# Performance work log

Hardware: AMD Instinct MI355X
Metric: run time of the kernel (lower is better)

The kernel has to match this reference:

```python
import jax, jax.numpy as jnp
import numpy as np

N_A, N_G, D, H = 100000, 25000, 128, 4
E_B, E_O, E_R, E_P = 400000, 100000, 200000, 200000
BN_INV = float(1.0 / np.sqrt(1.0 + 1e-5))  # eval-mode BatchNorm1d, running mean 0 / var 1


def setup_inputs():
    key = jax.random.key(0)
    ks = iter(jax.random.split(key, 64))
    nrm = lambda shape, s=0.05: jax.random.normal(next(ks), shape, jnp.float32) * s
    ri = lambda n, hi: jax.random.randint(next(ks), (n,), 0, hi, jnp.int32)
    inp = dict(
        x_atom=nrm((N_A, D), 1.0), x_group=nrm((N_G, D), 1.0),
        ef_bond=nrm((E_B, D), 1.0), ef_overlap=nrm((E_O, D), 1.0),
        bond_src=ri(E_B, N_A), bond_dst=ri(E_B, N_A),
        ov_src=ri(E_O, N_G), ov_dst=ri(E_O, N_G),
        ref_src=ri(E_R, N_G), ref_dst=ri(E_R, N_A),
        pool_src=ri(E_P, N_A), pool_dst=ri(E_P, N_G),
    )
    # two GINE convs (bond 'b', overlap 'o'): eps + MLP Linear(D,2D)->BN->ReLU->Linear(2D,D)
    for pre in ('b', 'o'):
        inp[pre + '_eps'] = jnp.zeros((1,), jnp.float32)
        inp[pre + '_W1'] = nrm((D, 2 * D)); inp[pre + '_b1'] = jnp.zeros((2 * D,), jnp.float32)
        inp[pre + '_g1'] = jnp.ones((2 * D,), jnp.float32); inp[pre + '_be1'] = jnp.zeros((2 * D,), jnp.float32)
        inp[pre + '_W2'] = nrm((2 * D, D)); inp[pre + '_b2'] = jnp.zeros((D,), jnp.float32)
    # two ModifiedGATConvs (refine 'r', pool 'p'): GATConv + Flatten->BN->ReLU->Linear
    for pre in ('r', 'p'):
        inp[pre + '_Wfc'] = nrm((D, H * D)); inp[pre + '_al'] = nrm((H, D)); inp[pre + '_ar'] = nrm((H, D))
        inp[pre + '_Wres'] = nrm((D, H * D)); inp[pre + '_bias'] = jnp.zeros((H * D,), jnp.float32)
        inp[pre + '_g'] = jnp.ones((H * D,), jnp.float32); inp[pre + '_b'] = jnp.zeros((H * D,), jnp.float32)
        inp[pre + '_Wout'] = nrm((H * D, D)); inp[pre + '_bout'] = jnp.zeros((D,), jnp.float32)
    return inp


def _gine(x_src, x_dst, efeat, src, dst, n_dst, eps, W1, b1, g1, be1, W2, b2):
    m = jax.nn.relu(x_src[src] + efeat)                       # [E, D] message: relu(h_src + e)
    neigh = jax.ops.segment_sum(m, dst, num_segments=n_dst)   # [Nd, D] sum-reduce
    h = (1.0 + eps) * x_dst + neigh
    h = h @ W1 + b1
    h = jax.nn.relu(g1 * (h * BN_INV) + be1)                  # eval BN
    return h @ W2 + b2


def _gat(x_src, x_dst, src, dst, n_dst, Wfc, al, ar, Wres, bias, g, b, Wout, bout):
    hs = (x_src @ Wfc).reshape(-1, H, D)                      # [Ns, H, D]
    hd = (x_dst @ Wfc).reshape(-1, H, D)
    el = jnp.sum(hs * al, axis=-1)                            # [Ns, H]
    er = jnp.sum(hd * ar, axis=-1)                            # [Nd, H]
    e = jax.nn.leaky_relu(el[src] + er[dst], 0.2)             # [E, H]
    emax = jax.ops.segment_max(e, dst, num_segments=n_dst)    # per-dst softmax (stable)
    ex = jnp.exp(e - emax[dst])
    den = jax.ops.segment_sum(ex, dst, num_segments=n_dst)
    a = ex / jnp.maximum(den[dst], 1e-9)                      # [E, H]
    rst = jax.ops.segment_sum(a[:, :, None] * hs[src], dst, num_segments=n_dst)  # [Nd, H, D]
    rst = rst + (x_dst @ Wres).reshape(-1, H, D) + bias.reshape(H, D)            # residual + bias
    flat = rst.reshape(-1, H * D)                             # Flatten
    h = jax.nn.relu(g * (flat * BN_INV) + b)                  # eval BN -> ReLU
    return h @ Wout + bout


def reference(x_atom, x_group, ef_bond, ef_overlap, bond_src, bond_dst, ov_src, ov_dst, ref_src, ref_dst, pool_src, pool_dst, b_eps, b_W1, b_b1, b_g1, b_be1, b_W2, b_b2, o_eps, o_W1, o_b1, o_g1, o_be1, o_W2, o_b2, r_Wfc, r_al, r_ar, r_Wres, r_bias, r_g, r_b, r_Wout, r_bout, p_Wfc, p_al, p_ar, p_Wres, p_bias, p_g, p_b, p_Wout, p_bout):
    # HeteroGraphConv with default 'sum' cross-relation aggregation per dst node type
    out_atom = _gine(x_atom, x_atom, ef_bond, bond_src, bond_dst, N_A, b_eps, b_W1, b_b1, b_g1, b_be1, b_W2, b_b2)
    out_atom = out_atom + _gat(x_group, x_atom, ref_src, ref_dst, N_A, r_Wfc, r_al, r_ar, r_Wres, r_bias, r_g, r_b, r_Wout, r_bout)
    out_group = _gine(x_group, x_group, ef_overlap, ov_src, ov_dst, N_G, o_eps, o_W1, o_b1, o_g1, o_be1, o_W2, o_b2)
    out_group = out_group + _gat(x_atom, x_group, pool_src, pool_dst, N_G, p_Wfc, p_al, p_ar, p_Wres, p_bias, p_g, p_b, p_Wout, p_bout)
    return jnp.concatenate([out_atom, out_group], axis=0)     # [N_A + N_G, D]
```

## Files before the change

kernel.cpp:

```cpp
#include <hip/hip_runtime.h>
#include <hip/hip_bf16.h>

#define N_A 100000
#define N_G 25000
#define DD 128
#define E_B 400000
#define E_O 100000
#define E_R 200000
#define E_P 200000
#define EALL 900000
#define NSLOT 250000
#define STRIDE 64

static constexpr float BN_INV_C = 0.99999500003749969f;

typedef __attribute__((ext_vector_type(8))) short bf16x8;
typedef __attribute__((ext_vector_type(4))) float f32x4;

__device__ __forceinline__ unsigned short f2bf(float f) {
    unsigned u = __float_as_uint(f);
    unsigned r = (u + 0x7FFFu + ((u >> 16) & 1u)) >> 16;
    return (unsigned short)r;
}
__device__ __forceinline__ float bf2f(unsigned short s) {
    return __uint_as_float(((unsigned)s) << 16);
}
__device__ __forceinline__ float lrelu(float v) { return v > 0.f ? v : 0.2f * v; }

__global__ void k_xcast_all(const float* __restrict__ xa, const float* __restrict__ xg,
                            unsigned short* __restrict__ xab, unsigned short* __restrict__ xgb) {
    int t = blockIdx.x * blockDim.x + threadIdx.x;
    if (t < N_A * 32) {
        float4 v = *(const float4*)(xa + (size_t)t * 4);
        ushort4 o; o.x = f2bf(v.x); o.y = f2bf(v.y); o.z = f2bf(v.z); o.w = f2bf(v.w);
        *(ushort4*)(xab + (size_t)t * 4) = o;
    } else {
        int t2 = t - N_A * 32;
        if (t2 >= N_G * 32) return;
        float4 v = *(const float4*)(xg + (size_t)t2 * 4);
        ushort4 o; o.x = f2bf(v.x); o.y = f2bf(v.y); o.z = f2bf(v.z); o.w = f2bf(v.w);
        *(ushort4*)(xgb + (size_t)t2 * 4) = o;
    }
}

struct WcSeg { const float* src; unsigned short* dst; int K; int N; int ldk; int off; };
struct WcArgs { WcSeg s[10]; };

__global__ void k_wcast_all(WcArgs a) {
    WcSeg sg = a.s[blockIdx.y];
    int t = blockIdx.x * blockDim.x + threadIdx.x;
    if (t >= sg.K * sg.N) return;
    int n = t % sg.N, k = t / sg.N;
    sg.dst[(size_t)n * sg.ldk + sg.off + k] = f2bf(sg.src[t]);
}

__global__ void k_war_all(const float* __restrict__ rWfc, const float* __restrict__ ral,
                          const float* __restrict__ rar, const float* __restrict__ pWfc,
                          const float* __restrict__ pal, const float* __restrict__ par,
                          float* __restrict__ wv) {
    int bsel = blockIdx.x;
    const float* W = bsel < 2 ? rWfc : pWfc;
    const float* vec = bsel == 0 ? ral : bsel == 1 ? rar : bsel == 2 ? pal : par;
    float* o = wv + bsel * 512;
    int t = threadIdx.x;
    int k = t >> 2, h = t & 3;
    const float* wr = W + (size_t)k * 512 + h * 128;
    const float* av = vec + h * 128;
    float s = 0.f;
    for (int d = 0; d < 128; ++d) s += wr[d] * av[d];
    o[t] = s;
}

__global__ void k_adj_fill(const int* __restrict__ bs, const int* __restrict__ bd,
                           const int* __restrict__ os, const int* __restrict__ od,
                           const int* __restrict__ rs, const int* __restrict__ rd,
                           const int* __restrict__ ps, const int* __restrict__ pd,
                           int* __restrict__ deg, uint2* __restrict__ adj,
                           int* __restrict__ heads, int* __restrict__ nxt) {
    int t = blockIdx.x * blockDim.x + threadIdx.x;
    int e, base, go; const int* S; const int* D;
    if (t < E_B) { e = t; S = bs; D = bd; base = 0; go = 0; }
    else if (t < E_B + E_O) { e = t - E_B; S = os; D = od; base = 100000; go = E_B; }
    else if (t < E_B + E_O + E_R) { e = t - (E_B + E_O); S = rs; D = rd; base = 125000; go = E_B + E_O; }
    else if (t < EALL) { e = t - (E_B + E_O + E_R); S = ps; D = pd; base = 225000; go = E_B + E_O + E_R; }
    else return;
    int d = D[e], s = S[e];
    int ns = base + d;
    int pos = atomicAdd(&deg[ns], 1);
    if (pos < STRIDE) adj[(size_t)ns * STRIDE + pos] = make_uint2((unsigned)e, (unsigned)s);
    else nxt[go + e] = atomicExch(&heads[ns], e);
}

__global__ __launch_bounds__(256) void k_gine_gather_all(
    const unsigned short* __restrict__ xAb, const unsigned short* __restrict__ xGb,
    const float* __restrict__ efB, const float* __restrict__ efO,
    const int* __restrict__ bsrc, const int* __restrict__ osrc,
    const int* __restrict__ deg, const uint2* __restrict__ adj,
    const int* __restrict__ heads, const int* __restrict__ nxt,
    const float* __restrict__ beps, const float* __restrict__ oeps,
    unsigned short* __restrict__ h0A, unsigned short* __restrict__ h0G) {
    int wid = threadIdx.x >> 6, lane = threadIdx.x & 63;
    int n = blockIdx.x * 4 + wid;
    __shared__ uint2 gl[4][STRIDE];
    const unsigned short* xs; const unsigned short* xdrow; const float* ef;
    const int* esrc; const int* nx; float ep; unsigned short* outp; int nn, base, go;
    if (n < N_A) {
        nn = n; xs = xAb; xdrow = xAb + (size_t)n * DD; ef = efB; esrc = bsrc;
        base = 0; go = 0; ep = 1.0f + beps[0]; outp = h0A + (size_t)n * DD;
    } else {
        nn = n - N_A; xs = xGb; xdrow = xGb + (size_t)nn * DD; ef = efO; esrc = osrc;
        base = 100000; go = E_B; ep = 1.0f + oeps[0]; outp = h0G + (size_t)nn * DD;
    }
    nx = nxt + go;
    int d = deg[base + nn];
    int cb = min(d, STRIDE);
    if (lane < cb) gl[wid][lane] = adj[(size_t)(base + nn) * STRIDE + lane];
    __syncthreads();
    float2 acc = make_float2(0.f, 0.f);
    for (int i = 0; i < cb; ++i) {
        uint2 es = gl[wid][i];
        unsigned xa = *(const unsigned*)(xs + (size_t)es.y * DD + lane * 2);
        float2 ev = *(const float2*)(ef + (size_t)es.x * DD + lane * 2);
        acc.x += fmaxf(bf2f((unsigned short)(xa & 0xffff)) + ev.x, 0.f);
        acc.y += fmaxf(bf2f((unsigned short)(xa >> 16)) + ev.y, 0.f);
    }
    if (d > STRIDE) {
        for (int e = heads[base + nn]; e >= 0; e = nx[e]) {
            int s = esrc[e];
            unsigned xa = *(const unsigned*)(xs + (size_t)s * DD + lane * 2);
            float2 ev = *(const float2*)(ef + (size_t)e * DD + lane * 2);
            acc.x += fmaxf(bf2f((unsigned short)(xa & 0xffff)) + ev.x, 0.f);
            acc.y += fmaxf(bf2f((unsigned short)(xa >> 16)) + ev.y, 0.f);
        }
    }
    unsigned xd = *(const unsigned*)(xdrow + lane * 2);
    float rx = ep * bf2f((unsigned short)(xd & 0xffff)) + acc.x;
    float ry = ep * bf2f((unsigned short)(xd >> 16)) + acc.y;
    *(unsigned*)(outp + lane * 2) = (unsigned)f2bf(rx) | ((unsigned)f2bf(ry) << 16);
}

__global__ void k_logit_all(const unsigned short* __restrict__ xAb,
                            const unsigned short* __restrict__ xGb,
                            const float* __restrict__ wv,
                            float* __restrict__ elR, float* __restrict__ elP,
                            float* __restrict__ erR, float* __restrict__ erP) {
    int t = blockIdx.x * blockDim.x + threadIdx.x;
    const unsigned short* xr; const float* wl; const float* wr_; float* ol; float* orr; int idx;
    if (t < N_A * 4) {
        idx = t; xr = xAb + (size_t)(t >> 2) * DD; wl = wv + 1024; wr_ = wv + 512;
        ol = elP; orr = erR;
    } else {
        int t2 = t - N_A * 4;
        if (t2 >= N_G * 4) return;
        idx = t2; xr = xGb + (size_t)(t2 >> 2) * DD; wl = wv; wr_ = wv + 1536;
        ol = elR; orr = erP;
    }
    int h = idx & 3;
    float sl = 0.f, sr = 0.f;
#pragma unroll
    for (int k = 0; k < DD; k += 8) {
        uint4 w = *(const uint4*)(xr + k);
        unsigned wa[4] = {w.x, w.y, w.z, w.w};
#pragma unroll
        for (int q = 0; q < 4; ++q) {
            float x0 = bf2f((unsigned short)(wa[q] & 0xffff));
            float x1 = bf2f((unsigned short)(wa[q] >> 16));
            int k0 = (k + q * 2) * 4 + h, k1 = (k + q * 2 + 1) * 4 + h;
            sl += x0 * wl[k0] + x1 * wl[k1];
            sr += x0 * wr_[k0] + x1 * wr_[k1];
        }
    }
    ol[idx] = sl;
    orr[idx] = sr;
}

__global__ void k_exp_all(const float* __restrict__ elR, const float* __restrict__ erR,
                          const float* __restrict__ elP, const float* __restrict__ erP,
                          const int* __restrict__ rs, const int* __restrict__ rd,
                          const int* __restrict__ ps, const int* __restrict__ pd,
                          float* __restrict__ exR, float* __restrict__ exP,
                          float* __restrict__ denR, float* __restrict__ denP) {
    int t = blockIdx.x * blockDim.x + threadIdx.x;
    if (t < E_R * 4) {
        int e = t >> 2, h = t & 3;
        float v = lrelu(elR[rs[e] * 4 + h] + erR[rd[e] * 4 + h]);
        float x = __expf(v);
        exR[t] = x;
        atomicAdd(&denR[rd[e] * 4 + h], x);
    } else {
        int t2 = t - E_R * 4;
        if (t2 >= E_P * 4) return;
        int e = t2 >> 2, h = t2 & 3;
        float v = lrelu(elP[ps[e] * 4 + h] + erP[pd[e] * 4 + h]);
        float x = __expf(v);
        exP[t2] = x;
        atomicAdd(&denP[pd[e] * 4 + h], x);
    }
}

__global__ __launch_bounds__(256) void k_att_gather_all(
    const unsigned short* __restrict__ xAb, const unsigned short* __restrict__ xGb,
    const float* __restrict__ exR, const float* __restrict__ exP,
    const float* __restrict__ denR, const float* __restrict__ denP,
    const int* __restrict__ rsrc, const int* __restrict__ psrc,
    const int* __restrict__ deg, const uint2* __restrict__ adj,
    const int* __restrict__ heads, const int* __restrict__ nxt,
    unsigned short* __restrict__ A2r, unsigned short* __restrict__ A2p) {
    int wid = threadIdx.x >> 6, lane = threadIdx.x & 63;
    int n = blockIdx.x * 4 + wid;
    __shared__ uint2 gl[4][STRIDE];
    const unsigned short* xs; const float* ex; const float* den;
    const int* esrc; const int* nx; unsigned short* A2; int nn, base, go;
    if (n < N_A) {
        nn = n; xs = xGb; ex = exR; den = denR; esrc = rsrc;
        base = 125000; go = E_B + E_O; A2 = A2r + (size_t)n * 512;
    } else {
        nn = n - N_A; xs = xAb; ex = exP; den = denP; esrc = psrc;
        base = 225000; go = E_B + E_O + E_R; A2 = A2p + (size_t)nn * 512;
    }
    nx = nxt + go;
    int d = deg[base + nn];
    int cb = min(d, STRIDE);
    if (lane < cb) gl[wid][lane] = adj[(size_t)(base + nn) * STRIDE + lane];
    __syncthreads();
    float4 dv = *(const float4*)(den + (size_t)nn * 4);
    float inv0 = 1.f / fmaxf(dv.x, 1e-9f);
    float inv1 = 1.f / fmaxf(dv.y, 1e-9f);
    float inv2 = 1.f / fmaxf(dv.z, 1e-9f);
    float inv3 = 1.f / fmaxf(dv.w, 1e-9f);
    float acc[4][2] = {};
    for (int i = 0; i < cb; ++i) {
        uint2 es = gl[wid][i];
        float4 e4 = *(const float4*)(ex + (size_t)es.x * 4);
        unsigned xw = *(const unsigned*)(xs + (size_t)es.y * DD + lane * 2);
        float x0 = bf2f((unsigned short)(xw & 0xffff));
        float x1 = bf2f((unsigned short)(xw >> 16));
        float a0 = e4.x * inv0, a1 = e4.y * inv1, a2 = e4.z * inv2, a3 = e4.w * inv3;
        acc[0][0] += a0 * x0; acc[0][1] += a0 * x1;
        acc[1][0] += a1 * x0; acc[1][1] += a1 * x1;
        acc[2][0] += a2 * x0; acc[2][1] += a2 * x1;
        acc[3][0] += a3 * x0; acc[3][1] += a3 * x1;
    }
    if (d > STRIDE) {
        for (int e = heads[base + nn]; e >= 0; e = nx[e]) {
            int s = esrc[e];
            float4 e4 = *(const float4*)(ex + (size_t)e * 4);
            unsigned xw = *(const unsigned*)(xs + (size_t)s * DD + lane * 2);
            float x0 = bf2f((unsigned short)(xw & 0xffff));
            float x1 = bf2f((unsigned short)(xw >> 16));
            float a0 = e4.x * inv0, a1 = e4.y * inv1, a2 = e4.z * inv2, a3 = e4.w * inv3;
            acc[0][0] += a0 * x0; acc[0][1] += a0 * x1;
            acc[1][0] += a1 * x0; acc[1][1] += a1 * x1;
            acc[2][0] += a2 * x0; acc[2][1] += a2 * x1;
            acc[3][0] += a3 * x0; acc[3][1] += a3 * x1;
        }
    }
#pragma unroll
    for (int h = 0; h < 4; ++h) {
        unsigned o = (unsigned)f2bf(acc[h][0]) | ((unsigned)f2bf(acc[h][1]) << 16);
        *(unsigned*)(A2 + h * 128 + lane * 2) = o;
    }
}

#define LDKP 40
template <int EPI, int OUTBF, int GATK>
__global__ __launch_bounds__(256) void k_gemm_bf(
    const unsigned short* __restrict__ A, const unsigned short* __restrict__ Bt,
    void* __restrict__ C, int M, int N, int K,
    const float* __restrict__ bias, const float* __restrict__ g,
    const float* __restrict__ be, const unsigned short* __restrict__ addbf,
    const unsigned short* __restrict__ Axd) {
    __shared__ unsigned short As[128 * LDKP];
    __shared__ unsigned short Bs[128 * LDKP];
    int tid = threadIdx.x;
    int wave = tid >> 6, lane = tid & 63;
    int wr = wave >> 1, wc = wave & 1;
    int row0 = blockIdx.y * 128, col0 = blockIdx.x * 128;
    int l16 = lane & 15, khalf = (lane >> 4) * 8;
    f32x4 acc[4][4] = {};
    int r_0 = tid >> 2, ko_0 = (tid & 3) * 8;
    int r_1 = (tid + 256) >> 2, ko_1 = ((tid + 256) & 3) * 8;
    for (int k0 = 0; k0 < K; k0 += 32) {
        __syncthreads();
        {
            int kk = k0 + ko_0;
            int ra = min(row0 + r_0, M - 1);
            uint4 va;
            if (GATK) va = (kk < 128) ? *(const uint4*)(A + (size_t)ra * 512 + col0 + kk)
                                      : *(const uint4*)(Axd + (size_t)ra * 128 + (kk - 128));
            else va = *(const uint4*)(A + (size_t)ra * K + kk);
            *(uint4*)(&As[r_0 * LDKP + ko_0]) = va;
            uint4 vb = *(const uint4*)(Bt + (size_t)(col0 + r_0) * K + kk);
            *(uint4*)(&Bs[r_0 * LDKP + ko_0]) = vb;
            kk = k0 + ko_1;
            ra = min(row0 + r_1, M - 1);
            if (GATK) va = (kk < 128) ? *(const uint4*)(A + (size_t)ra * 512 + col0 + kk)
                                      : *(const uint4*)(Axd + (size_t)ra * 128 + (kk - 128));
            else va = *(const uint4*)(A + (size_t)ra * K + kk);
            *(uint4*)(&As[r_1 * LDKP + ko_1]) = va;
            vb = *(const uint4*)(Bt + (size_t)(col0 + r_1) * K + kk);
            *(uint4*)(&Bs[r_1 * LDKP + ko_1]) = vb;
        }
        __syncthreads();
        bf16x8 af[4], bfr[4];
#pragma unroll
        for (int i = 0; i < 4; ++i)
            af[i] = *(const bf16x8*)(&As[(wr * 64 + i * 16 + l16) * LDKP + khalf]);
#pragma unroll
        for (int j = 0; j < 4; ++j)
            bfr[j] = *(const bf16x8*)(&Bs[(wc * 64 + j * 16 + l16) * LDKP + khalf]);
#pragma unroll
        for (int i = 0; i < 4; ++i)
#pragma unroll
            for (int j = 0; j < 4; ++j)
                acc[i][j] = __builtin_amdgcn_mfma_f32_16x16x32_bf16(af[i], bfr[j], acc[i][j], 0, 0, 0);
    }
    int rq = (lane >> 4) * 4;
#pragma unroll
    for (int i = 0; i < 4; ++i) {
#pragma unroll
        for (int reg = 0; reg < 4; ++reg) {
            int r = row0 + wr * 64 + i * 16 + rq + reg;
            if (r >= M) continue;
#pragma unroll
            for (int j = 0; j < 4; ++j) {
                int c = col0 + wc * 64 + j * 16 + l16;
                float v = acc[i][j][reg];
                size_t idx = (size_t)r * N + c;
                v += bias[c];
                if (EPI == 2) {
                    v = g[c] * (v * BN_INV_C) + be[c];
                    v = fmaxf(v, 0.f);
                }
                if (EPI == 3) {
                    ((float*)C)[idx] = v + bf2f(addbf[idx]);
                } else if (OUTBF) {
                    ((unsigned short*)C)[idx] = f2bf(v);
                } else {
                    ((float*)C)[idx] = v;
                }
            }
        }
    }
}

extern "C" void kernel_launch(void* const* d_in, const int* in_sizes, int n_in,
                              void* d_out, int out_size, void* d_ws, size_t ws_size,
                              hipStream_t stream) {
    const float* x_atom = (const float*)d_in[0];
    const float* x_group = (const float*)d_in[1];
    const float* ef_bond = (const float*)d_in[2];
    const float* ef_ov = (const float*)d_in[3];
    const int* bond_src = (const int*)d_in[4];
    const int* bond_dst = (const int*)d_in[5];
    const int* ov_src = (const int*)d_in[6];
    const int* ov_dst = (const int*)d_in[7];
    const int* ref_src = (const int*)d_in[8];
    const int* ref_dst = (const int*)d_in[9];
    const int* pool_src = (const int*)d_in[10];
    const int* pool_dst = (const int*)d_in[11];
    const float* b_eps = (const float*)d_in[12];
    const float* b_W1 = (const float*)d_in[13];
    const float* b_b1 = (const float*)d_in[14];
    const float* b_g1 = (const float*)d_in[15];
    const float* b_be1 = (const float*)d_in[16];
    const float* b_W2 = (const float*)d_in[17];
    const float* b_b2 = (const float*)d_in[18];
    const float* o_eps = (const float*)d_in[19];
    const float* o_W1 = (const float*)d_in[20];
    const float* o_b1 = (const float*)d_in[21];
    const float* o_g1 = (const float*)d_in[22];
    const float* o_be1 = (const float*)d_in[23];
    const float* o_W2 = (const float*)d_in[24];
    const float* o_b2 = (const float*)d_in[25];
    const float* r_Wfc = (const float*)d_in[26];
    const float* r_al = (const float*)d_in[27];
    const float* r_ar = (const float*)d_in[28];
    const float* r_Wres = (const float*)d_in[29];
    const float* r_bias = (const float*)d_in[30];
    const float* r_g = (const float*)d_in[31];
    const float* r_b = (const float*)d_in[32];
    const float* r_Wout = (const float*)d_in[33];
    const float* r_bout = (const float*)d_in[34];
    const float* p_Wfc = (const float*)d_in[35];
    const float* p_al = (const float*)d_in[36];
    const float* p_ar = (const float*)d_in[37];
    const float* p_Wres = (const float*)d_in[38];
    const float* p_bias = (const float*)d_in[39];
    const float* p_g = (const float*)d_in[40];
    const float* p_b = (const float*)d_in[41];
    const float* p_Wout = (const float*)d_in[42];
    const float* p_bout = (const float*)d_in[43];

    float* out = (float*)d_out;
    char* wsb = (char*)d_ws;
    unsigned short* xAb = (unsigned short*)(wsb + 0);
    unsigned short* xGb = (unsigned short*)(wsb + 26000000);
    unsigned short* WtB1 = (unsigned short*)(wsb + 33000000);
    unsigned short* WtB2 = WtB1 + 32768;
    unsigned short* WtO1 = WtB2 + 32768;
    unsigned short* WtO2 = WtO1 + 32768;
    unsigned short* WtR  = WtO2 + 32768;
    unsigned short* WtRo = WtR + 131072;
    unsigned short* WtP  = WtRo + 65536;
    unsigned short* WtPo = WtP + 131072;
    float* wv   = (float*)(wsb + 34100000);
    int* heads  = (int*)(wsb + 36300000);
    int* nxt    = (int*)(wsb + 37400000);
    unsigned short* h0A = (unsigned short*)(wsb + 41100000);
    unsigned short* h0G = (unsigned short*)(wsb + 66800000);
    unsigned short* R4  = (unsigned short*)(wsb + 73300000);
    unsigned short* G1a = (unsigned short*)(wsb + 124600000);
    unsigned short* G1g = (unsigned short*)(wsb + 150300000);
    unsigned short* A2r = (unsigned short*)(wsb + 156800000);
    unsigned short* A2p = (unsigned short*)(wsb + 259300000);
    unsigned short* R3r = (unsigned short*)(wsb + 285000000);
    unsigned short* R3p = (unsigned short*)(wsb + 387500000);
    uint2* adj  = (uint2*)(wsb + 414000000);
    int* deg    = (int*)(wsb + 543000000);
    float* F    = (float*)(wsb + 544000000);
    float* elR  = F;
    float* elP  = F + 100000;
    float* erR  = F + 500000;
    float* erP  = F + 900000;
    float* denR = F + 1000000;
    float* denP = F + 1400000;
    float* exR  = F + 1500000;
    float* exP  = F + 2300000;

    k_xcast_all<<<((N_A + N_G) * 32 + 255) / 256, 256, 0, stream>>>(x_atom, x_group, xAb, xGb);
    WcArgs wa;
    wa.s[0] = {b_W1, WtB1, 128, 256, 128, 0};
    wa.s[1] = {b_W2, WtB2, 256, 128, 256, 0};
    wa.s[2] = {o_W1, WtO1, 128, 256, 128, 0};
    wa.s[3] = {o_W2, WtO2, 256, 128, 256, 0};
    wa.s[4] = {r_Wfc, WtR, 128, 512, 256, 0};
    wa.s[5] = {r_Wres, WtR, 128, 512, 256, 128};
    wa.s[6] = {r_Wout, WtRo, 512, 128, 512, 0};
    wa.s[7] = {p_Wfc, WtP, 128, 512, 256, 0};
    wa.s[8] = {p_Wres, WtP, 128, 512, 256, 128};
    wa.s[9] = {p_Wout, WtPo, 512, 128, 512, 0};
    k_wcast_all<<<dim3(256, 10), 256, 0, stream>>>(wa);
    k_war_all<<<4, 512, 0, stream>>>(r_Wfc, r_al, r_ar, p_Wfc, p_al, p_ar, wv);
    hipMemsetAsync(deg, 0, NSLOT * 4, stream);
    hipMemsetAsync(heads, 0xFF, NSLOT * 4, stream);
    hipMemsetAsync(denR, 0, 500000 * 4, stream);
    k_adj_fill<<<(EALL + 255) / 256, 256, 0, stream>>>(
        bond_src, bond_dst, ov_src, ov_dst, ref_src, ref_dst, pool_src, pool_dst,
        deg, adj, heads, nxt);
    k_gine_gather_all<<<31250, 256, 0, stream>>>(xAb, xGb, ef_bond, ef_ov, bond_src, ov_src,
                                                 deg, adj, heads, nxt, b_eps, o_eps, h0A, h0G);
    k_gemm_bf<2, 1, 0><<<dim3(2, 782), 256, 0, stream>>>(h0A, WtB1, R4, N_A, 256, 128, b_b1, b_g1, b_be1, nullptr, nullptr);
    k_gemm_bf<1, 1, 0><<<dim3(1, 782), 256, 0, stream>>>(R4, WtB2, G1a, N_A, 128, 256, b_b2, nullptr, nullptr, nullptr, nullptr);
    k_gemm_bf<2, 1, 0><<<dim3(2, 196), 256, 0, stream>>>(h0G, WtO1, R4, N_G, 256, 128, o_b1, o_g1, o_be1, nullptr, nullptr);
    k_gemm_bf<1, 1, 0><<<dim3(1, 196), 256, 0, stream>>>(R4, WtO2, G1g, N_G, 128, 256, o_b2, nullptr, nullptr, nullptr, nullptr);
    k_logit_all<<<((N_A + N_G) * 4 + 255) / 256, 256, 0, stream>>>(xAb, xGb, wv, elR, elP, erR, erP);
    k_exp_all<<<((E_R + E_P) * 4 + 255) / 256, 256, 0, stream>>>(elR, erR, elP, erP,
        ref_src, ref_dst, pool_src, pool_dst, exR, exP, denR, denP);
    k_att_gather_all<<<31250, 256, 0, stream>>>(xAb, xGb, exR, exP, denR, denP, ref_src, pool_src,
                                                deg, adj, heads, nxt, A2r, A2p);
    k_gemm_bf<2, 1, 1><<<dim3(4, 782), 256, 0, stream>>>(A2r, WtR, R3r, N_A, 512, 256, r_bias, r_g, r_b, nullptr, xAb);
    k_gemm_bf<2, 1, 1><<<dim3(4, 196), 256, 0, stream>>>(A2p, WtP, R3p, N_G, 512, 256, p_bias, p_g, p_b, nullptr, xGb);
    k_gemm_bf<3, 0, 0><<<dim3(1, 782), 256, 0, stream>>>(R3r, WtRo, out, N_A, 128, 512, r_bout, nullptr, nullptr, G1a, nullptr);
    k_gemm_bf<3, 0, 0><<<dim3(1, 196), 256, 0, stream>>>(R3p, WtPo, out + (size_t)N_A * DD, N_G, 128, 512, p_bout, nullptr, nullptr, G1g, nullptr);
}
```

Measured before the change: 596.8 us.

## Merge independent kernels into fewer grouped launches and batch GEMMs

Combines the casting, weight transpose, attention-vector precompute and adjacency fill into one prep kernel, fuses the GINE gather with the logit computation, and groups the GEMMs into three launches that dispatch sub-problems by block index. A separate R4g buffer lets the group-side GEMMs run alongside the atom-side ones. The aim is to cut launch count and fill tail idle time. The cost is heavier kernels with more branching, and possibly higher register pressure from the shared gemm_body.

Measured after the change: 542.3 us. -9.1%, faster.

```diff
diff --git a/kernel.cpp b/kernel.cpp
--- a/kernel.cpp
+++ b/kernel.cpp
@@ -27,151 +27,156 @@
 }
 __device__ __forceinline__ float lrelu(float v) { return v > 0.f ? v : 0.2f * v; }
 
-__global__ void k_xcast_all(const float* __restrict__ xa, const float* __restrict__ xg,
-                            unsigned short* __restrict__ xab, unsigned short* __restrict__ xgb) {
-    int t = blockIdx.x * blockDim.x + threadIdx.x;
-    if (t < N_A * 32) {
-        float4 v = *(const float4*)(xa + (size_t)t * 4);
-        ushort4 o; o.x = f2bf(v.x); o.y = f2bf(v.y); o.z = f2bf(v.z); o.w = f2bf(v.w);
-        *(ushort4*)(xab + (size_t)t * 4) = o;
+struct WcSeg { const float* src; unsigned short* dst; int K; int N; int ldk; int off; };
+struct PrepArgs {
+    const float* xa; const float* xg;
+    unsigned short* xab; unsigned short* xgb;
+    WcSeg wc[10];
+    const float* rWfc; const float* ral; const float* rar;
+    const float* pWfc; const float* pal; const float* par;
+    float* wv;
+    const int* bs; const int* bd; const int* os; const int* od;
+    const int* rs; const int* rd; const int* ps; const int* pd;
+    int* deg; uint2* adj; int* heads; int* nxt;
+};
+
+#define PB_XC 15625
+#define PB_WC 2560
+#define PB_WAR 8
+
+__global__ __launch_bounds__(256) void k_prep(PrepArgs p) {
+    int bx = blockIdx.x, tid = threadIdx.x;
+    if (bx < PB_XC) {
+        int t = bx * 256 + tid;
+        if (t < N_A * 32) {
+            float4 v = *(const float4*)(p.xa + (size_t)t * 4);
+            ushort4 o; o.x = f2bf(v.x); o.y = f2bf(v.y); o.z = f2bf(v.z); o.w = f2bf(v.w);
+            *(ushort4*)(p.xab + (size_t)t * 4) = o;
+        } else {
+            int t2 = t - N_A * 32;
+            if (t2 < N_G * 32) {
+                float4 v = *(const float4*)(p.xg + (size_t)t2 * 4);
+                ushort4 o; o.x = f2bf(v.x); o.y = f2bf(v.y); o.z = f2bf(v.z); o.w = f2bf(v.w);
+                *(ushort4*)(p.xgb + (size_t)t2 * 4) = o;
+            }
+        }
+    } else if (bx < PB_XC + PB_WC) {
+        int b2 = bx - PB_XC;
+        WcSeg sg = p.wc[b2 >> 8];
+        int t = ((b2 & 255) << 8) + tid;
+        if (t < sg.K * sg.N) {
+            int n = t % sg.N, k = t / sg.N;
+            sg.dst[(size_t)n * sg.ldk + sg.off + k] = f2bf(sg.src[t]);
+        }
+    } else if (bx < PB_XC + PB_WC + PB_WAR) {
+        int b3 = bx - (PB_XC + PB_WC);
+        int bsel = b3 >> 1;
+        int t = ((b3 & 1) << 8) + tid;
+        const float* W = bsel < 2 ? p.rWfc : p.pWfc;
+        const float* vec = bsel == 0 ? p.ral : bsel == 1 ? p.rar : bsel == 2 ? p.pal : p.par;
+        int k = t >> 2, h = t & 3;
+        const float* wr = W + (size_t)k * 512 + h * 128;
+        const float* av = vec + h * 128;
+        float s = 0.f;
+        for (int d = 0; d < 128; ++d) s += wr[d] * av[d];
+        p.wv[bsel * 512 + t] = s;
     } else {
-        int t2 = t - N_A * 32;
-        if (t2 >= N_G * 32) return;
-        float4 v = *(const float4*)(xg + (size_t)t2 * 4);
-        ushort4 o; o.x = f2bf(v.x); o.y = f2bf(v.y); o.z = f2bf(v.z); o.w = f2bf(v.w);
-        *(ushort4*)(xgb + (size_t)t2 * 4) = o;
-    }
-}
-
-struct WcSeg { const float* src; unsigned short* dst; int K; int N; int ldk; int off; };
-struct WcArgs { WcSeg s[10]; };
-
-__global__ void k_wcast_all(WcArgs a) {
-    WcSeg sg = a.s[blockIdx.y];
-    int t = blockIdx.x * blockDim.x + threadIdx.x;
-    if (t >= sg.K * sg.N) return;
-    int n = t % sg.N, k = t / sg.N;
-    sg.dst[(size_t)n * sg.ldk + sg.off + k] = f2bf(sg.src[t]);
-}
-
-__global__ void k_war_all(const float* __restrict__ rWfc, const float* __restrict__ ral,
-                          const float* __restrict__ rar, const float* __restrict__ pWfc,
-                          const float* __restrict__ pal, const float* __restrict__ par,
-                          float* __restrict__ wv) {
-    int bsel = blockIdx.x;
-    const float* W = bsel < 2 ? rWfc : pWfc;
-    const float* vec = bsel == 0 ? ral : bsel == 1 ? rar : bsel == 2 ? pal : par;
-    float* o = wv + bsel * 512;
-    int t = threadIdx.x;
-    int k = t >> 2, h = t & 3;
-    const float* wr = W + (size_t)k * 512 + h * 128;
-    const float* av = vec + h * 128;
-    float s = 0.f;
-    for (int d = 0; d < 128; ++d) s += wr[d] * av[d];
-    o[t] = s;
-}
-
-__global__ void k_adj_fill(const int* __restrict__ bs, const int* __restrict__ bd,
-                           const int* __restrict__ os, const int* __restrict__ od,
-                           const int* __restrict__ rs, const int* __restrict__ rd,
-                           const int* __restrict__ ps, const int* __restrict__ pd,
-                           int* __restrict__ deg, uint2* __restrict__ adj,
-                           int* __restrict__ heads, int* __restrict__ nxt) {
-    int t = blockIdx.x * blockDim.x + threadIdx.x;
-    int e, base, go; const int* S; const int* D;
-    if (t < E_B) { e = t; S = bs; D = bd; base = 0; go = 0; }
-    else if (t < E_B + E_O) { e = t - E_B; S = os; D = od; base = 100000; go = E_B; }
-    else if (t < E_B + E_O + E_R) { e = t - (E_B + E_O); S = rs; D = rd; base = 125000; go = E_B + E_O; }
-    else if (t < EALL) { e = t - (E_B + E_O + E_R); S = ps; D = pd; base = 225000; go = E_B + E_O + E_R; }
-    else return;
-    int d = D[e], s = S[e];
-    int ns = base + d;
-    int pos = atomicAdd(&deg[ns], 1);
-    if (pos < STRIDE) adj[(size_t)ns * STRIDE + pos] = make_uint2((unsigned)e, (unsigned)s);
-    else nxt[go + e] = atomicExch(&heads[ns], e);
-}
-
-__global__ __launch_bounds__(256) void k_gine_gather_all(
+        int t = (bx - (PB_XC + PB_WC + PB_WAR)) * 256 + tid;
+        int e, base, go; const int* S; const int* D;
+        if (t < E_B) { e = t; S = p.bs; D = p.bd; base = 0; go = 0; }
+        else if (t < E_B + E_O) { e = t - E_B; S = p.os; D = p.od; base = 100000; go = E_B; }
+        else if (t < E_B + E_O + E_R) { e = t - (E_B + E_O); S = p.rs; D = p.rd; base = 125000; go = E_B + E_O; }
+        else if (t < EALL) { e = t - (E_B + E_O + E_R); S = p.ps; D = p.pd; base = 225000; go = E_B + E_O + E_R; }
+        else return;
+        int d = D[e], s = S[e];
+        int ns = base + d;
+        int pos = atomicAdd(&p.deg[ns], 1);
+        if (pos < STRIDE) p.adj[(size_t)ns * STRIDE + pos] = make_uint2((unsigned)e, (unsigned)s);
+        else p.nxt[go + e] = atomicExch(&p.heads[ns], e);
+    }
+}
+
+__global__ __launch_bounds__(256) void k_gather_logit(
     const unsigned short* __restrict__ xAb, const unsigned short* __restrict__ xGb,
     const float* __restrict__ efB, const float* __restrict__ efO,
     const int* __restrict__ bsrc, const int* __restrict__ osrc,
     const int* __restrict__ deg, const uint2* __restrict__ adj,
     const int* __restrict__ heads, const int* __restrict__ nxt,
     const float* __restrict__ beps, const float* __restrict__ oeps,
-    unsigned short* __restrict__ h0A, unsigned short* __restrict__ h0G) {
-    int wid = threadIdx.x >> 6, lane = threadIdx.x & 63;
-    int n = blockIdx.x * 4 + wid;
+    unsigned short* __restrict__ h0A, unsigned short* __restrict__ h0G,
+    const float* __restrict__ wv,
+    float* __restrict__ elR, float* __restrict__ elP,
+    float* __restrict__ erR, float* __restrict__ erP) {
     __shared__ uint2 gl[4][STRIDE];
-    const unsigned short* xs; const unsigned short* xdrow; const float* ef;
-    const int* esrc; const int* nx; float ep; unsigned short* outp; int nn, base, go;
-    if (n < N_A) {
-        nn = n; xs = xAb; xdrow = xAb + (size_t)n * DD; ef = efB; esrc = bsrc;
-        base = 0; go = 0; ep = 1.0f + beps[0]; outp = h0A + (size_t)n * DD;
-    } else {
-        nn = n - N_A; xs = xGb; xdrow = xGb + (size_t)nn * DD; ef = efO; esrc = osrc;
-        base = 100000; go = E_B; ep = 1.0f + oeps[0]; outp = h0G + (size_t)nn * DD;
-    }
-    nx = nxt + go;
-    int d = deg[base + nn];
-    int cb = min(d, STRIDE);
-    if (lane < cb) gl[wid][lane] = adj[(size_t)(base + nn) * STRIDE + lane];
-    __syncthreads();
-    float2 acc = make_float2(0.f, 0.f);
-    for (int i = 0; i < cb; ++i) {
-        uint2 es = gl[wid][i];
-        unsigned xa = *(const unsigned*)(xs + (size_t)es.y * DD + lane * 2);
-        float2 ev = *(const float2*)(ef + (size_t)es.x * DD + lane * 2);
-        acc.x += fmaxf(bf2f((unsigned short)(xa & 0xffff)) + ev.x, 0.f);
-        acc.y += fmaxf(bf2f((unsigned short)(xa >> 16)) + ev.y, 0.f);
-    }
-    if (d > STRIDE) {
-        for (int e = heads[base + nn]; e >= 0; e = nx[e]) {
-            int s = esrc[e];
-            unsigned xa = *(const unsigned*)(xs + (size_t)s * DD + lane * 2);
-            float2 ev = *(const float2*)(ef + (size_t)e * DD + lane * 2);
+    int bx = blockIdx.x;
+    if (bx < 31250) {
+        int wid = threadIdx.x >> 6, lane = threadIdx.x & 63;
+        int n = bx * 4 + wid;
+        const unsigned short* xs; const unsigned short* xdrow; const float* ef;
+        const int* esrc; const int* nx; float ep; unsigned short* outp; int nn, base, go;
+        if (n < N_A) {
+            nn = n; xs = xAb; xdrow = xAb + (size_t)n * DD; ef = efB; esrc = bsrc;
+            base = 0; go = 0; ep = 1.0f + beps[0]; outp = h0A + (size_t)n * DD;
+        } else {
+            nn = n - N_A; xs = xGb; xdrow = xGb + (size_t)nn * DD; ef = efO; esrc = osrc;
+            base = 100000; go = E_B; ep = 1.0f + oeps[0]; outp = h0G + (size_t)nn * DD;
+        }
+        nx = nxt + go;
+        int d = deg[base + nn];
+        int cb = min(d, STRIDE);
+        if (lane < cb) gl[wid][lane] = adj[(size_t)(base + nn) * STRIDE + lane];
+        __syncthreads();
+        float2 acc = make_float2(0.f, 0.f);
+        for (int i = 0; i < cb; ++i) {
+            uint2 es = gl[wid][i];
+            unsigned xa = *(const unsigned*)(xs + (size_t)es.y * DD + lane * 2);
+            float2 ev = *(const float2*)(ef + (size_t)es.x * DD + lane * 2);
             acc.x += fmaxf(bf2f((unsigned short)(xa & 0xffff)) + ev.x, 0.f);
             acc.y += fmaxf(bf2f((unsigned short)(xa >> 16)) + ev.y, 0.f);
         }
-    }
-    unsigned xd = *(const unsigned*)(xdrow + lane * 2);
-    float rx = ep * bf2f((unsigned short)(xd & 0xffff)) + acc.x;
-    float ry = ep * bf2f((unsigned short)(xd >> 16)) + acc.y;
-    *(unsigned*)(outp + lane * 2) = (unsigned)f2bf(rx) | ((unsigned)f2bf(ry) << 16);
-}
-
-__global__ void k_logit_all(const unsigned short* __restrict__ xAb,
-                            const unsigned short* __restrict__ xGb,
-                            const float* __restrict__ wv,
-                            float* __restrict__ elR, float* __restrict__ elP,
-                            float* __restrict__ erR, float* __restrict__ erP) {
-    int t = blockIdx.x * blockDim.x + threadIdx.x;
-    const unsigned short* xr; const float* wl; const float* wr_; float* ol; float* orr; int idx;
-    if (t < N_A * 4) {
-        idx = t; xr = xAb + (size_t)(t >> 2) * DD; wl = wv + 1024; wr_ = wv + 512;
-        ol = elP; orr = erR;
+        if (d > STRIDE) {
+            for (int e = heads[base + nn]; e >= 0; e = nx[e]) {
+                int s = esrc[e];
+                unsigned xa = *(const unsigned*)(xs + (size_t)s * DD + lane * 2);
+                float2 ev = *(const float2*)(ef + (size_t)e * DD + lane * 2);
+                acc.x += fmaxf(bf2f((unsigned short)(xa & 0xffff)) + ev.x, 0.f);
+                acc.y += fmaxf(bf2f((unsigned short)(xa >> 16)) + ev.y, 0.f);
+            }
+        }
+        unsigned xd = *(const unsigned*)(xdrow + lane * 2);
+        float rx = ep * bf2f((unsigned short)(xd & 0xffff)) + acc.x;
+        float ry = ep * bf2f((unsigned short)(xd >> 16)) + acc.y;
+        *(unsigned*)(outp + lane * 2) = (unsigned)f2bf(rx) | ((unsigned)f2bf(ry) << 16);
     } else {
-        int t2 = t - N_A * 4;
-        if (t2 >= N_G * 4) return;
-        idx = t2; xr = xGb + (size_t)(t2 >> 2) * DD; wl = wv; wr_ = wv + 1536;
-        ol = elR; orr = erP;
-    }
-    int h = idx & 3;
-    float sl = 0.f, sr = 0.f;
-#pragma unroll
-    for (int k = 0; k < DD; k += 8) {
-        uint4 w = *(const uint4*)(xr + k);
-        unsigned wa[4] = {w.x, w.y, w.z, w.w};
-#pragma unroll
-        for (int q = 0; q < 4; ++q) {
-            float x0 = bf2f((unsigned short)(wa[q] & 0xffff));
-            float x1 = bf2f((unsigned short)(wa[q] >> 16));
-            int k0 = (k + q * 2) * 4 + h, k1 = (k + q * 2 + 1) * 4 + h;
-            sl += x0 * wl[k0] + x1 * wl[k1];
-            sr += x0 * wr_[k0] + x1 * wr_[k1];
-        }
-    }
-    ol[idx] = sl;
-    orr[idx] = sr;
+        int t = (bx - 31250) * 256 + threadIdx.x;
+        const unsigned short* xr; const float* wl; const float* wr_; float* ol; float* orr; int idx;
+        if (t < N_A * 4) {
+            idx = t; xr = xAb + (size_t)(t >> 2) * DD; wl = wv + 1024; wr_ = wv + 512;
+            ol = elP; orr = erR;
+        } else {
+            int t2 = t - N_A * 4;
+            if (t2 >= N_G * 4) return;
+            idx = t2; xr = xGb + (size_t)(t2 >> 2) * DD; wl = wv; wr_ = wv + 1536;
+            ol = elR; orr = erP;
+        }
+        int h = idx & 3;
+        float sl = 0.f, sr = 0.f;
+#pragma unroll
+        for (int k = 0; k < DD; k += 8) {
+            uint4 w = *(const uint4*)(xr + k);
+            unsigned wa[4] = {w.x, w.y, w.z, w.w};
+#pragma unroll
+            for (int q = 0; q < 4; ++q) {
+                float x0 = bf2f((unsigned short)(wa[q] & 0xffff));
+                float x1 = bf2f((unsigned short)(wa[q] >> 16));
+                int k0 = (k + q * 2) * 4 + h, k1 = (k + q * 2 + 1) * 4 + h;
+                sl += x0 * wl[k0] + x1 * wl[k1];
+                sr += x0 * wr_[k0] + x1 * wr_[k1];
+            }
+        }
+        ol[idx] = sl;
+        orr[idx] = sr;
+    }
 }
 
 __global__ void k_exp_all(const float* __restrict__ elR, const float* __restrict__ erR,
@@ -264,42 +269,40 @@
 
 #define LDKP 40
 template <int EPI, int OUTBF, int GATK>
-__global__ __launch_bounds__(256) void k_gemm_bf(
+__device__ __forceinline__ void gemm_body(
     const unsigned short* __restrict__ A, const unsigned short* __restrict__ Bt,
     void* __restrict__ C, int M, int N, int K,
     const float* __restrict__ bias, const float* __restrict__ g,
     const float* __restrict__ be, const unsigned short* __restrict__ addbf,
-    const unsigned short* __restrict__ Axd) {
-    __shared__ unsigned short As[128 * LDKP];
-    __shared__ unsigned short Bs[128 * LDKP];
+    const unsigned short* __restrict__ Axd, int bxx, int byy,
+    unsigned short* As, unsigned short* Bs) {
     int tid = threadIdx.x;
     int wave = tid >> 6, lane = tid & 63;
     int wr = wave >> 1, wc = wave & 1;
-    int row0 = blockIdx.y * 128, col0 = blockIdx.x * 128;
+    int row0 = byy * 128, col0 = bxx * 128;
     int l16 = lane & 15, khalf = (lane >> 4) * 8;
     f32x4 acc[4][4] = {};
-    int r_0 = tid >> 2, ko_0 = (tid & 3) * 8;
-    int r_1 = (tid + 256) >> 2, ko_1 = ((tid + 256) & 3) * 8;
+    int r_0 = tid >> 2, ko = (tid & 3) * 8;
+    int r_1 = r_0 + 64;
     for (int k0 = 0; k0 < K; k0 += 32) {
         __syncthreads();
         {
-            int kk = k0 + ko_0;
+            int kk = k0 + ko;
             int ra = min(row0 + r_0, M - 1);
             uint4 va;
             if (GATK) va = (kk < 128) ? *(const uint4*)(A + (size_t)ra * 512 + col0 + kk)
                                       : *(const uint4*)(Axd + (size_t)ra * 128 + (kk - 128));
             else va = *(const uint4*)(A + (size_t)ra * K + kk);
-            *(uint4*)(&As[r_0 * LDKP + ko_0]) = va;
+            *(uint4*)(&As[r_0 * LDKP + ko]) = va;
             uint4 vb = *(const uint4*)(Bt + (size_t)(col0 + r_0) * K + kk);
-            *(uint4*)(&Bs[r_0 * LDKP + ko_0]) = vb;
-            kk = k0 + ko_1;
+            *(uint4*)(&Bs[r_0 * LDKP + ko]) = vb;
             ra = min(row0 + r_1, M - 1);
             if (GATK) va = (kk < 128) ? *(const uint4*)(A + (size_t)ra * 512 + col0 + kk)
                                       : *(const uint4*)(Axd + (size_t)ra * 128 + (kk - 128));
             else va = *(const uint4*)(A + (size_t)ra * K + kk);
-            *(uint4*)(&As[r_1 * LDKP + ko_1]) = va;
+            *(uint4*)(&As[r_1 * LDKP + ko]) = va;
             vb = *(const uint4*)(Bt + (size_t)(col0 + r_1) * K + kk);
-            *(uint4*)(&Bs[r_1 * LDKP + ko_1]) = vb;
+            *(uint4*)(&Bs[r_1 * LDKP + ko]) = vb;
         }
         __syncthreads();
         bf16x8 af[4], bfr[4];
@@ -342,6 +345,76 @@
             }
         }
     }
+}
+
+#define NBA 782
+#define NBG 196
+
+__global__ __launch_bounds__(256) void k_gemm1(
+    const unsigned short* h0A, const unsigned short* h0G,
+    const unsigned short* WtB1, const unsigned short* WtO1,
+    const float* bb1, const float* bg1, const float* bbe1,
+    const float* ob1, const float* og1, const float* obe1,
+    unsigned short* R4a, unsigned short* R4g) {
+    __shared__ unsigned short As[128 * LDKP];
+    __shared__ unsigned short Bs[128 * LDKP];
+    int b = blockIdx.x;
+    if (b < 2 * NBA)
+        gemm_body<2, 1, 0>(h0A, WtB1, R4a, N_A, 256, 128, bb1, bg1, bbe1, nullptr, nullptr,
+                           b & 1, b >> 1, As, Bs);
+    else {
+        int b2 = b - 2 * NBA;
+        gemm_body<2, 1, 0>(h0G, WtO1, R4g, N_G, 256, 128, ob1, og1, obe1, nullptr, nullptr,
+                           b2 & 1, b2 >> 1, As, Bs);
+    }
+}
+
+__global__ __launch_bounds__(256) void k_gemm_mid(
+    const unsigned short* R4a, const unsigned short* R4g,
+    const unsigned short* WtB2, const unsigned short* WtO2,
+    const float* bb2, const float* ob2,
+    unsigned short* G1a, unsigned short* G1g,
+    const unsigned short* A2r, const unsigned short* A2p,
+    const unsigned short* xAb, const unsigned short* xGb,
+    const unsigned short* WtR, const unsigned short* WtP,
+    const float* rbias, const float* rg, const float* rb,
+    const float* pbias, const float* pg, const float* pb,
+    unsigned short* R3r, unsigned short* R3p) {
+    __shared__ unsigned short As[128 * LDKP];
+    __shared__ unsigned short Bs[128 * LDKP];
+    int b = blockIdx.x;
+    if (b < NBA)
+        gemm_body<1, 1, 0>(R4a, WtB2, G1a, N_A, 128, 256, bb2, nullptr, nullptr, nullptr, nullptr,
+                           0, b, As, Bs);
+    else if (b < NBA + NBG)
+        gemm_body<1, 1, 0>(R4g, WtO2, G1g, N_G, 128, 256, ob2, nullptr, nullptr, nullptr, nullptr,
+                           0, b - NBA, As, Bs);
+    else if (b < NBA + NBG + 4 * NBA) {
+        int b3 = b - (NBA + NBG);
+        gemm_body<2, 1, 1>(A2r, WtR, R3r, N_A, 512, 256, rbias, rg, rb, nullptr, xAb,
+                           b3 & 3, b3 >> 2, As, Bs);
+    } else {
+        int b4 = b - (NBA + NBG + 4 * NBA);
+        gemm_body<2, 1, 1>(A2p, WtP, R3p, N_G, 512, 256, pbias, pg, pb, nullptr, xGb,
+                           b4 & 3, b4 >> 2, As, Bs);
+    }
+}
+
+__global__ __launch_bounds__(256) void k_gemm_out(
+    const unsigned short* R3r, const unsigned short* R3p,
+    const unsigned short* WtRo, const unsigned short* WtPo,
+    const float* rbout, const float* pbout,
+    const unsigned short* G1a, const unsigned short* G1g,
+    float* out) {
+    __shared__ unsigned short As[128 * LDKP];
+    __shared__ unsigned short Bs[128 * LDKP];
+    int b = blockIdx.x;
+    if (b < NBA)
+        gemm_body<3, 0, 0>(R3r, WtRo, out, N_A, 128, 512, rbout, nullptr, nullptr, G1a, nullptr,
+                           0, b, As, Bs);
+    else
+        gemm_body<3, 0, 0>(R3p, WtPo, out + (size_t)N_A * DD, N_G, 128, 512, pbout, nullptr, nullptr,
+                           G1g, nullptr, 0, b - NBA, As, Bs);
 }
 
 extern "C" void kernel_launch(void* const* d_in, const int* in_sizes, int n_in,
@@ -409,7 +482,7 @@
     int* nxt    = (int*)(wsb + 37400000);
     unsigned short* h0A = (unsigned short*)(wsb + 41100000);
     unsigned short* h0G = (unsigned short*)(wsb + 66800000);
-    unsigned short* R4  = (unsigned short*)(wsb + 73300000);
+    unsigned short* R4a = (unsigned short*)(wsb + 73300000);
     unsigned short* G1a = (unsigned short*)(wsb + 124600000);
     unsigned short* G1g = (unsigned short*)(wsb + 150300000);
     unsigned short* A2r = (unsigned short*)(wsb + 156800000);
@@ -427,40 +500,49 @@
     float* denP = F + 1400000;
     float* exR  = F + 1500000;
     float* exP  = F + 2300000;
-
-    k_xcast_all<<<((N_A + N_G) * 32 + 255) / 256, 256, 0, stream>>>(x_atom, x_group, xAb, xGb);
-    WcArgs wa;
-    wa.s[0] = {b_W1, WtB1, 128, 256, 128, 0};
-    wa.s[1] = {b_W2, WtB2, 256, 128, 256, 0};
-    wa.s[2] = {o_W1, WtO1, 128, 256, 128, 0};
-    wa.s[3] = {o_W2, WtO2, 256, 128, 256, 0};
-    wa.s[4] = {r_Wfc, WtR, 128, 512, 256, 0};
-    wa.s[5] = {r_Wres, WtR, 128, 512, 256, 128};
-    wa.s[6] = {r_Wout, WtRo, 512, 128, 512, 0};
-    wa.s[7] = {p_Wfc, WtP, 128, 512, 256, 0};
-    wa.s[8] = {p_Wres, WtP, 128, 512, 256, 128};
-    wa.s[9] = {p_Wout, WtPo, 512, 128, 512, 0};
-    k_wcast_all<<<dim3(256, 10), 256, 0, stream>>>(wa);
-    k_war_all<<<4, 512, 0, stream>>>(r_Wfc, r_al, r_ar, p_Wfc, p_al, p_ar, wv);
+    unsigned short* R4g = (unsigned short*)(wsb + 560000000);
+
     hipMemsetAsync(deg, 0, NSLOT * 4, stream);
     hipMemsetAsync(heads, 0xFF, NSLOT * 4, stream);
     hipMemsetAsync(denR, 0, 500000 * 4, stream);
-    k_adj_fill<<<(EALL + 255) / 256, 256, 0, stream>>>(
-        bond_src, bond_dst, ov_src, ov_dst, ref_src, ref_dst, pool_src, pool_dst,
-        deg, adj, heads, nxt);
-    k_gine_gather_all<<<31250, 256, 0, stream>>>(xAb, xGb, ef_bond, ef_ov, bond_src, ov_src,
-                                                 deg, adj, heads, nxt, b_eps, o_eps, h0A, h0G);
-    k_gemm_bf<2, 1, 0><<<dim3(2, 782), 256, 0, stream>>>(h0A, WtB1, R4, N_A, 256, 128, b_b1, b_g1, b_be1, nullptr, nullptr);
-    k_gemm_bf<1, 1, 0><<<dim3(1, 782), 256, 0, stream>>>(R4, WtB2, G1a, N_A, 128, 256, b_b2, nullptr, nullptr, nullptr, nullptr);
-    k_gemm_bf<2, 1, 0><<<dim3(2, 196), 256, 0, stream>>>(h0G, WtO1, R4, N_G, 256, 128, o_b1, o_g1, o_be1, nullptr, nullptr);
-    k_gemm_bf<1, 1, 0><<<dim3(1, 196), 256, 0, stream>>>(R4, WtO2, G1g, N_G, 128, 256, o_b2, nullptr, nullptr, nullptr, nullptr);
-    k_logit_all<<<((N_A + N_G) * 4 + 255) / 256, 256, 0, stream>>>(xAb, xGb, wv, elR, elP, erR, erP);
-    k_exp_all<<<((E_R + E_P) * 4 + 255) / 256, 256, 0, stream>>>(elR, erR, elP, erP,
+
+    PrepArgs pa;
+    pa.xa = x_atom; pa.xg = x_group; pa.xab = xAb; pa.xgb = xGb;
+    pa.wc[0] = {b_W1, WtB1, 128, 256, 128, 0};
+    pa.wc[1] = {b_W2, WtB2, 256, 128, 256, 0};
+    pa.wc[2] = {o_W1, WtO1, 128, 256, 128, 0};
+    pa.wc[3] = {o_W2, WtO2, 256, 128, 256, 0};
+    pa.wc[4] = {r_Wfc, WtR, 128, 512, 256, 0};
+    pa.wc[5] = {r_Wres, WtR, 128, 512, 256, 128};
+    pa.wc[6] = {r_Wout, WtRo, 512, 128, 512, 0};
+    pa.wc[7] = {p_Wfc, WtP, 128, 512, 256, 0};
+    pa.wc[8] = {p_Wres, WtP, 128, 512, 256, 128};
+    pa.wc[9] = {p_Wout, WtPo, 512, 128, 512, 0};
+    pa.rWfc = r_Wfc; pa.ral = r_al; pa.rar = r_ar;
+    pa.pWfc = p_Wfc; pa.pal = p_al; pa.par = p_ar; pa.wv = wv;
+    pa.bs = bond_src; pa.bd = bond_dst; pa.os = ov_src; pa.od = ov_dst;
+    pa.rs = ref_src; pa.rd = ref_dst; pa.ps = pool_src; pa.pd = pool_dst;
+    pa.deg = deg; pa.adj = adj; pa.heads = heads; pa.nxt = nxt;
+    k_prep<<<PB_XC + PB_WC + PB_WAR + 3516, 256, 0, stream>>>(pa);
+
+    k_gather_logit<<<31250 + 1954, 256, 0, stream>>>(
+        xAb, xGb, ef_bond, ef_ov, bond_src, ov_src, deg, adj, heads, nxt,
+        b_eps, o_eps, h0A, h0G, wv, elR, elP, erR, erP);
+
+    k_exp_all<<<6250, 256, 0, stream>>>(elR, erR, elP, erP,
         ref_src, ref_dst, pool_src, pool_dst, exR, exP, denR, denP);
+
+    k_gemm1<<<2 * NBA + 2 * NBG, 256, 0, stream>>>(h0A, h0G, WtB1, WtO1,
+        b_b1, b_g1, b_be1, o_b1, o_g1, o_be1, R4a, R4g);
+
     k_att_gather_all<<<31250, 256, 0, stream>>>(xAb, xGb, exR, exP, denR, denP, ref_src, pool_src,
                                                 deg, adj, heads, nxt, A2r, A2p);
-    k_gemm_bf<2, 1, 1><<<dim3(4, 782), 256, 0, stream>>>(A2r, WtR, R3r, N_A, 512, 256, r_bias, r_g, r_b, nullptr, xAb);
-    k_gemm_bf<2, 1, 1><<<dim3(4, 196), 256, 0, stream>>>(A2p, WtP, R3p, N_G, 512, 256, p_bias, p_g, p_b, nullptr, xGb);
-    k_gemm_bf<3, 0, 0><<<dim3(1, 782), 256, 0, stream>>>(R3r, WtRo, out, N_A, 128, 512, r_bout, nullptr, nullptr, G1a, nullptr);
-    k_gemm_bf<3, 0, 0><<<dim3(1, 196), 256, 0, stream>>>(R3p, WtPo, out + (size_t)N_A * DD, N_G, 128, 512, p_bout, nullptr, nullptr, G1g, nullptr);
-}
+
+    k_gemm_mid<<<NBA + NBG + 4 * NBA + 4 * NBG, 256, 0, stream>>>(
+        R4a, R4g, WtB2, WtO2, b_b2, o_b2, G1a, G1g,
+        A2r, A2p, xAb, xGb, WtR, WtP,
+        r_bias, r_g, r_b, p_bias, p_g, p_b, R3r, R3p);
+
+    k_gemm_out<<<NBA + NBG, 256, 0, stream>>>(R3r, R3p, WtRo, WtPo, r_bout, p_bout,
+                                              G1a, G1g, out);
+}
```
